# Performance work log

Hardware: AMD Instinct MI355X
Metric: run time of the kernel (lower is better)

## Reference

```python
import jax, jax.numpy as jnp
import numpy as np

H = 1024
HEADS = 16
FFN = 4096
EPS = 1e-5


def _layernorm(x, g, b):
    mu = jnp.mean(x, axis=-1, keepdims=True)
    var = jnp.mean((x - mu) ** 2, axis=-1, keepdims=True)
    return (x - mu) * jax.lax.rsqrt(var + EPS) * g + b


def setup_inputs() -> dict:
    key = jax.random.key(0)
    ks = jax.random.split(key, 12)
    N, L = 2, 2048
    s = 1.0 / np.sqrt(H)
    inp = {
        "src_hidden": jax.random.normal(ks[0], (N, L, H), dtype=jnp.float32),
        "key_mask": jnp.ones((N, L), dtype=jnp.int32),
        "Wq": jax.random.normal(ks[1], (H, H), dtype=jnp.float32) * s,
        "bq": jnp.zeros((H,), dtype=jnp.float32),
        "Wk": jax.random.normal(ks[2], (H, H), dtype=jnp.float32) * s,
        "bk": jnp.zeros((H,), dtype=jnp.float32),
        "Wv": jax.random.normal(ks[3], (H, H), dtype=jnp.float32) * s,
        "bv": jnp.zeros((H,), dtype=jnp.float32),
        "Wo": jax.random.normal(ks[4], (H, H), dtype=jnp.float32) * s,
        "bo": jnp.zeros((H,), dtype=jnp.float32),
        "ln1_g": jnp.ones((H,), dtype=jnp.float32),
        "ln1_b": jnp.zeros((H,), dtype=jnp.float32),
        "W1": jax.random.normal(ks[5], (H, FFN), dtype=jnp.float32) * s,
        "b1": jnp.zeros((FFN,), dtype=jnp.float32),
        "W2": jax.random.normal(ks[6], (FFN, H), dtype=jnp.float32) * (1.0 / np.sqrt(FFN)),
        "b2": jnp.zeros((H,), dtype=jnp.float32),
        "ln2_g": jnp.ones((H,), dtype=jnp.float32),
        "ln2_b": jnp.zeros((H,), dtype=jnp.float32),
    }
    return inp


def reference(src_hidden, key_mask, Wq, bq, Wk, bk, Wv, bv, Wo, bo,
              ln1_g, ln1_b, W1, b1, W2, b2, ln2_g, ln2_b):
    N, L, _ = src_hidden.shape
    d = H // HEADS
    # projections -> (N, heads, L, d)
    q = (src_hidden @ Wq + bq).reshape(N, L, HEADS, d).transpose(0, 2, 1, 3)
    k = (src_hidden @ Wk + bk).reshape(N, L, HEADS, d).transpose(0, 2, 1, 3)
    v = (src_hidden @ Wv + bv).reshape(N, L, HEADS, d).transpose(0, 2, 1, 3)
    # faithful quirk: Q/=sqrt(H) and K/=sqrt(H)  =>  scores scaled by 1/H
    sims = jnp.einsum('bhid,bhjd->bhij', q, k) / H  # (N, heads, L, L)
    mask = key_mask[:, None, None, :] != 0          # (N,1,1,L), masked=False
    sims = jnp.where(mask, sims, -jnp.inf)
    attn = jax.nn.softmax(sims, axis=-1)
    ctx = jnp.einsum('bhij,bhjd->bhid', attn, v)
    concats = ctx.transpose(0, 2, 1, 3).reshape(N, L, H)
    mhsa = concats @ Wo + bo
    # residual + LN1
    x = _layernorm(mhsa + src_hidden, ln1_g, ln1_b)
    # FFN (dropout=0 / eval) + residual + LN2
    ffn = jax.nn.relu(x @ W1 + b1) @ W2 + b2
    out = _layernorm(ffn + x, ln2_g, ln2_b)
    return out
```

## Files before the change

kernel.cpp:

```cpp
#include <hip/hip_runtime.h>
#include <math.h>

#define Hd   1024
#define SEQL 2048
#define NB   2
#define NHEADS 16
#define FFND 4096
#define ROWS 4096
#define QKVLD 3072

typedef __attribute__((ext_vector_type(8))) short short8;
typedef __attribute__((ext_vector_type(4))) float f32x4;
typedef __attribute__((ext_vector_type(16))) float f32x16;

__device__ __forceinline__ unsigned short f2bf(float f) {
  union { float f; unsigned int u; } v; v.f = f;
  return (unsigned short)((v.u + 0x7fffu + ((v.u >> 16) & 1u)) >> 16);
}
__device__ __forceinline__ unsigned short f2bf_fast(float f) {
  union { float f; unsigned int u; } v; v.f = f;
  return (unsigned short)((v.u + 0x8000u) >> 16);
}
__device__ __forceinline__ float bf2f(unsigned short u) {
  union { unsigned int u; float f; } v; v.u = (unsigned int)u << 16;
  return v.f;
}
__device__ __forceinline__ int cvtpk(float a, float b) {
  int d;
  asm("v_cvt_pk_bf16_f32 %0, %1, %2" : "=v"(d) : "v"(a), "v"(b));
  return d;
}
__device__ __forceinline__ void pswap(int& a, int& b) {
  asm("v_permlane32_swap_b32 %0, %1" : "+v"(a), "+v"(b));
}

__device__ __forceinline__ void gl_lds16(const unsigned short* g,
                                         unsigned short* l) {
  __builtin_amdgcn_global_load_lds(
      (const __attribute__((address_space(1))) void*)g,
      (__attribute__((address_space(3))) void*)l, 16, 0, 0);
}

__global__ __launch_bounds__(256) void convert_bf16(
    const float* __restrict__ in, unsigned short* __restrict__ out,
    const float* __restrict__ a, const float* __restrict__ b,
    const float* __restrict__ c, float* __restrict__ o) {
  const int bid = blockIdx.x;
  if (bid >= ROWS * Hd / 1024) {
    const int i = (bid - ROWS * Hd / 1024) * 256 + threadIdx.x;
    o[i] = (i < 1024) ? a[i] : (i < 2048 ? b[i - 1024] : c[i - 2048]);
    return;
  }
  const int i = (bid * 256 + threadIdx.x) * 4;
  float4 x = *(const float4*)&in[i];
  ushort4 ov;
  ov.x = f2bf(x.x); ov.y = f2bf(x.y); ov.z = f2bf(x.z); ov.w = f2bf(x.w);
  *(ushort4*)&out[i] = ov;
}

__global__ __launch_bounds__(256) void convert_transpose(
    const float* __restrict__ W, int ld,
    unsigned short* __restrict__ Wt, int ldt) {
  __shared__ float T[64][65];
  const int t = threadIdx.x;
  const int c0 = blockIdx.x * 64, r0 = blockIdx.y * 64;
#pragma unroll
  for (int p = 0; p < 4; ++p) {
    const int lin = t + p * 256;
    const int r = lin >> 4, c4 = (lin & 15) * 4;
    float4 x = *(const float4*)&W[(size_t)(r0 + r) * ld + c0 + c4];
    T[r][c4 + 0] = x.x; T[r][c4 + 1] = x.y;
    T[r][c4 + 2] = x.z; T[r][c4 + 3] = x.w;
  }
  __syncthreads();
#pragma unroll
  for (int p = 0; p < 2; ++p) {
    const int lin = t + p * 256;
    const int oc = lin >> 3, ch = (lin & 7) * 8;
    union { unsigned short u[8]; uint4 v; } x;
#pragma unroll
    for (int i = 0; i < 8; ++i) x.u[i] = f2bf(T[ch + i][oc]);
    *(uint4*)&Wt[(size_t)(c0 + oc) * ldt + r0 + ch] = x.v;
  }
}

__global__ __launch_bounds__(256) void convert_transpose4(
    const float* __restrict__ W0, const float* __restrict__ W1,
    const float* __restrict__ W2, const float* __restrict__ W3,
    unsigned short* __restrict__ T0, unsigned short* __restrict__ T1,
    unsigned short* __restrict__ T2, unsigned short* __restrict__ T3) {
  __shared__ float T[64][65];
  const float* W = (blockIdx.z == 0) ? W0 : (blockIdx.z == 1) ? W1
                 : (blockIdx.z == 2) ? W2 : W3;
  unsigned short* Wt = (blockIdx.z == 0) ? T0 : (blockIdx.z == 1) ? T1
                     : (blockIdx.z == 2) ? T2 : T3;
  const int t = threadIdx.x;
  const int c0 = blockIdx.x * 64, r0 = blockIdx.y * 64;
#pragma unroll
  for (int p = 0; p < 4; ++p) {
    const int lin = t + p * 256;
    const int r = lin >> 4, c4 = (lin & 15) * 4;
    float4 x = *(const float4*)&W[(size_t)(r0 + r) * Hd + c0 + c4];
    T[r][c4 + 0] = x.x; T[r][c4 + 1] = x.y;
    T[r][c4 + 2] = x.z; T[r][c4 + 3] = x.w;
  }
  __syncthreads();
#pragma unroll
  for (int p = 0; p < 2; ++p) {
    const int lin = t + p * 256;
    const int oc = lin >> 3, ch = (lin & 7) * 8;
    union { unsigned short u[8]; uint4 v; } x;
#pragma unroll
    for (int i = 0; i < 8; ++i) x.u[i] = f2bf(T[ch + i][oc]);
    *(uint4*)&Wt[(size_t)(c0 + oc) * Hd + r0 + ch] = x.v;
  }
}

__global__ __launch_bounds__(256) void transpose_v(
    const unsigned short* __restrict__ v, unsigned short* __restrict__ vt) {
  __shared__ unsigned short T[64][72];
  const int t = threadIdx.x;
  const int s0 = (blockIdx.x & 31) * 64;
  const int bh = blockIdx.x >> 5;
  const int b = bh >> 4, h = bh & 15;
#pragma unroll
  for (int p = 0; p < 2; ++p) {
    const int lin = t + p * 256;
    const int r = lin >> 3, c8 = (lin & 7) * 8;
    *(uint4*)&T[r][c8] =
        *(const uint4*)&v[(size_t)(b * SEQL + s0 + r) * QKVLD + h * 64 + c8];
  }
  __syncthreads();
#pragma unroll
  for (int p = 0; p < 2; ++p) {
    const int lin = t + p * 256;
    const int d = lin >> 3, c8 = (lin & 7) * 8;
    union { unsigned short u[8]; uint4 v4; } x;
#pragma unroll
    for (int i = 0; i < 8; ++i) x.u[i] = T[c8 + i][d];
    *(uint4*)&vt[(size_t)(bh * 64 + d) * SEQL + s0 + c8] = x.v4;
  }
}

template <int BN, int MODE, int OUTBF>
__global__ __launch_bounds__(256, (BN == 128 ? 3 : 4)) void gemm_bt(
    const unsigned short* __restrict__ A, int lda,
    const unsigned short* __restrict__ Bt, int ldb,
    const float* __restrict__ bias,
    void* __restrict__ Cv, int ldc, int K) {
  constexpr int NI = (BN == 128) ? 4 : 2;
  constexpr int BG = BN / 32;
  __shared__ unsigned short As[128 * 64];
  __shared__ unsigned short Bs[BN * 64];
  const int t = threadIdx.x;
  const int wave = t >> 6, lane = t & 63;
  const int l16 = lane & 15, quad = lane >> 4;
  const int m0 = blockIdx.y * 128, n0 = blockIdx.x * BN;
  const int wm = (wave >> 1) * 64, wn = (wave & 1) * (BN / 2);

  const int lr8 = lane >> 3;
  const int sc8 = 8 * ((lane & 7) ^ lr8);

  f32x4 acc[4][NI];
#pragma unroll
  for (int i = 0; i < 4; ++i)
#pragma unroll
    for (int j = 0; j < NI; ++j) acc[i][j] = (f32x4){0.f, 0.f, 0.f, 0.f};

  const unsigned short* Apg[4];
  unsigned short* lAg[4];
#pragma unroll
  for (int j = 0; j < 4; ++j) {
    const int r0 = (wave + 4 * j) * 8;
    Apg[j] = &A[(size_t)(m0 + r0 + lr8) * lda + sc8];
    lAg[j] = &As[r0 * 64];
  }
  const unsigned short* Bpg[BG];
  unsigned short* lBg[BG];
#pragma unroll
  for (int j = 0; j < BG; ++j) {
    const int r0 = (wave + 4 * j) * 8;
    Bpg[j] = &Bt[(size_t)(n0 + r0 + lr8) * ldb + sc8];
    lBg[j] = &Bs[r0 * 64];
  }

  for (int k0 = 0; k0 < K; k0 += 64) {
#pragma unroll
    for (int j = 0; j < 4; ++j) gl_lds16(Apg[j] + k0, lAg[j]);
#pragma unroll
    for (int j = 0; j < BG; ++j) gl_lds16(Bpg[j] + k0, lBg[j]);
    __syncthreads();

#pragma unroll
    for (int kh = 0; kh < 2; ++kh) {
      short8 af[4], bfr[NI];
#pragma unroll
      for (int mi = 0; mi < 4; ++mi) {
        const int r = wm + mi * 16 + l16;
        af[mi] = *(const short8*)&As[r * 64 + (((quad + 4 * kh) ^ (r & 7)) * 8)];
      }
#pragma unroll
      for (int ni = 0; ni < NI; ++ni) {
        const int r = wn + ni * 16 + l16;
        bfr[ni] = *(const short8*)&Bs[r * 64 + (((quad + 4 * kh) ^ (r & 7)) * 8)];
      }
#pragma unroll
      for (int mi = 0; mi < 4; ++mi)
#pragma unroll
        for (int ni = 0; ni < NI; ++ni)
          acc[mi][ni] = __builtin_amdgcn_mfma_f32_16x16x32_bf16(
              af[mi], bfr[ni], acc[mi][ni], 0, 0, 0);
    }
    __syncthreads();
  }

#pragma unroll
  for (int mi = 0; mi < 4; ++mi) {
#pragma unroll
    for (int ni = 0; ni < NI; ++ni) {
      const int col = n0 + wn + ni * 16 + l16;
      const float bv = (MODE == 2) ? 0.0f : bias[col];
#pragma unroll
      for (int r = 0; r < 4; ++r) {
        const int row = m0 + wm + mi * 16 + quad * 4 + r;
        float v = acc[mi][ni][r] + bv;
        if (MODE == 1) v = fmaxf(v, 0.0f);
        if (OUTBF) {
          ((unsigned short*)Cv)[(size_t)row * ldc + col] = f2bf_fast(v);
        } else {
          float* Cf = (float*)Cv;
          if (MODE == 2) Cf[(size_t)row * ldc + col] += v;
          else           Cf[(size_t)row * ldc + col] = v;
        }
      }
    }
  }
}

__global__ __launch_bounds__(256, 4) void attn_mfma(
    const unsigned short* __restrict__ Q,
    const unsigned short* __restrict__ K,
    const unsigned short* __restrict__ Vt,
    const int* __restrict__ mask,
    unsigned short* __restrict__ Op,
    float* __restrict__ ls) {
  __shared__ unsigned short Ks[64 * 72];
  __shared__ unsigned short Vs[64 * 72];

  const int t = threadIdx.x;
  const int wave = t >> 6, lane = t & 63;
  const int l32 = lane & 31, hi = lane >> 5;
  const int qb = blockIdx.x & 15;
  const int h  = (blockIdx.x >> 4) & 15;
  const int b  = (blockIdx.x >> 8) & 1;
  const int jh = blockIdx.x >> 9;
  const int q0 = qb * 128;
  const int bh = b * NHEADS + h;
  const int jbeg = jh * (SEQL / 2), jend = jbeg + SEQL / 2;
  const float NEGINF = -__builtin_inff();

  const int lr = t >> 3, lc8 = (t & 7) * 8;
  const unsigned short* Kbase = &K[(size_t)(b * SEQL + lr) * QKVLD + h * 64 + lc8];
  const unsigned short* Vbase = &Vt[(size_t)(bh * 64 + lr) * SEQL + lc8];
  const size_t Krow32 = (size_t)32 * QKVLD;

  const unsigned short* Qrow =
      &Q[(size_t)(b * SEQL + q0 + wave * 32 + l32) * QKVLD + h * 64];
  short8 qf[4];
#pragma unroll
  for (int ks = 0; ks < 4; ++ks)
    qf[ks] = *(const short8*)&Qrow[ks * 16 + hi * 8];

  float lrow = 0.f;
  f32x16 accO[2];
#pragma unroll
  for (int dt = 0; dt < 2; ++dt)
#pragma unroll
    for (int r = 0; r < 16; ++r) accO[dt][r] = 0.f;

  uint4 kv0 = *(const uint4*)(Kbase + (size_t)jbeg * QKVLD);
  uint4 kv1 = *(const uint4*)(Kbase + (size_t)jbeg * QKVLD + Krow32);
  uint4 vv0 = *(const uint4*)(Vbase + jbeg);
  uint4 vv1 = *(const uint4*)(Vbase + jbeg + 32 * SEQL);

  for (int j0 = jbeg; j0 < jend; j0 += 64) {
    __syncthreads();
    *(uint4*)&Ks[lr * 72 + lc8] = kv0;
    *(uint4*)&Ks[(lr + 32) * 72 + lc8] = kv1;
    *(uint4*)&Vs[lr * 72 + lc8] = vv0;
    *(uint4*)&Vs[(lr + 32) * 72 + lc8] = vv1;
    __syncthreads();

    if (j0 + 64 < jend) {
      const unsigned short* kp = Kbase + (size_t)(j0 + 64) * QKVLD;
      const unsigned short* vp = Vbase + (j0 + 64);
      kv0 = *(const uint4*)(kp);
      kv1 = *(const uint4*)(kp + Krow32);
      vv0 = *(const uint4*)(vp);
      vv1 = *(const uint4*)(vp + 32 * SEQL);
    }

#pragma unroll
    for (int jt = 0; jt < 2; ++jt) {
      f32x16 z;
#pragma unroll
      for (int r = 0; r < 16; ++r) z[r] = 0.f;
#pragma unroll
      for (int ks = 0; ks < 4; ++ks) {
        const short8 ka =
            *(const short8*)&Ks[(jt * 32 + l32) * 72 + ks * 16 + hi * 8];
        z = __builtin_amdgcn_mfma_f32_32x32x16_bf16(ka, qf[ks], z, 0, 0, 0);
      }

      int pk[8];
#pragma unroll
      for (int g = 0; g < 4; ++g) {
        const int4 mm =
            *(const int4*)&mask[b * SEQL + j0 + jt * 32 + g * 8 + hi * 4];
        const int mr[4] = {mm.x, mm.y, mm.z, mm.w};
        float p[4];
#pragma unroll
        for (int e = 0; e < 4; ++e) {
          const float x = mr[e] ? z[g * 4 + e] * (1.0f / 1024.0f) : NEGINF;
          p[e] = __expf(x);
          lrow += p[e];
        }
        pk[g * 2 + 0] = cvtpk(p[0], p[1]);
        pk[g * 2 + 1] = cvtpk(p[2], p[3]);
      }
      pswap(pk[0], pk[2]); pswap(pk[1], pk[3]);
      pswap(pk[4], pk[6]); pswap(pk[5], pk[7]);
      union { int i[4]; short8 s; } pa0, pa1;
      pa0.i[0] = pk[0]; pa0.i[1] = pk[1]; pa0.i[2] = pk[2]; pa0.i[3] = pk[3];
      pa1.i[0] = pk[4]; pa1.i[1] = pk[5]; pa1.i[2] = pk[6]; pa1.i[3] = pk[7];

#pragma unroll
      for (int dt = 0; dt < 2; ++dt) {
        const short8 vb0 = *(const short8*)&Vs[(dt * 32 + l32) * 72 +
                                               jt * 32 + hi * 8];
        const short8 vb1 = *(const short8*)&Vs[(dt * 32 + l32) * 72 +
                                               jt * 32 + 16 + hi * 8];
        accO[dt] = __builtin_amdgcn_mfma_f32_32x32x16_bf16(pa0.s, vb0,
                                                           accO[dt], 0, 0, 0);
        accO[dt] = __builtin_amdgcn_mfma_f32_32x32x16_bf16(pa1.s, vb1,
                                                           accO[dt], 0, 0, 0);
      }
    }
  }

  lrow += __shfl_xor(lrow, 32);
  if (hi == 0)
    ls[((size_t)(jh * NB + b) * NHEADS + h) * SEQL + q0 + wave * 32 + l32] =
        lrow;

#pragma unroll
  for (int dt = 0; dt < 2; ++dt)
#pragma unroll
    for (int r = 0; r < 16; ++r) {
      const int qr = q0 + wave * 32 + (r & 3) + 8 * (r >> 2) + 4 * hi;
      const int rowg = b * SEQL + qr;
      Op[(size_t)jh * ROWS * Hd + (size_t)rowg * Hd + h * 64 + dt * 32 + l32] =
          f2bf_fast(accO[dt][r]);
    }
}

__global__ __launch_bounds__(256) void attn_combine(
    const unsigned short* __restrict__ Op, const float* __restrict__ ls,
    unsigned short* __restrict__ ctxb) {
  const int row = blockIdx.x;
  const int b = row >> 11, q = row & (SEQL - 1);
  const int t = threadIdx.x;
  const int c0 = t * 4, h = t >> 4;
  const float l0 = ls[((size_t)(b)*NHEADS + h) * SEQL + q];
  const float l1 = ls[((size_t)(NB + b) * NHEADS + h) * SEQL + q];
  const float inv = 1.0f / (l0 + l1);
  ushort4 a = *(const ushort4*)&Op[(size_t)row * Hd + c0];
  ushort4 c = *(const ushort4*)&Op[(size_t)ROWS * Hd + (size_t)row * Hd + c0];
  ushort4 o;
  o.x = f2bf_fast((bf2f(a.x) + bf2f(c.x)) * inv);
  o.y = f2bf_fast((bf2f(a.y) + bf2f(c.y)) * inv);
  o.z = f2bf_fast((bf2f(a.z) + bf2f(c.z)) * inv);
  o.w = f2bf_fast((bf2f(a.w) + bf2f(c.w)) * inv);
  *(ushort4*)&ctxb[(size_t)row * Hd + c0] = o;
}

template <int ABF>
__global__ __launch_bounds__(256) void add_ln_kernel(
    const void* Av, const float* R,
    const float* __restrict__ gamma, const float* __restrict__ beta,
    float* out, unsigned short* outb) {
  const int row = blockIdx.x;
  const int t = threadIdx.x;
  const size_t baser = (size_t)row * Hd;

  float a0, a1, a2, a3;
  if (ABF) {
    ushort4 a = *(const ushort4*)&((const unsigned short*)Av)[baser + t * 4];
    a0 = bf2f(a.x); a1 = bf2f(a.y); a2 = bf2f(a.z); a3 = bf2f(a.w);
  } else {
    float4 a = *(const float4*)&((const float*)Av)[baser + t * 4];
    a0 = a.x; a1 = a.y; a2 = a.z; a3 = a.w;
  }
  float4 r = *(const float4*)&R[baser + t * 4];
  float x0 = a0 + r.x, x1 = a1 + r.y, x2 = a2 + r.z, x3 = a3 + r.w;
  float s  = x0 + x1 + x2 + x3;
  float ss = x0 * x0 + x1 * x1 + x2 * x2 + x3 * x3;

#pragma unroll
  for (int off = 32; off > 0; off >>= 1) {
    s  += __shfl_down(s, off, 64);
    ss += __shfl_down(ss, off, 64);
  }

  __shared__ float rs[4], rss[4];
  __shared__ float sh_mean, sh_rstd;
  if ((t & 63) == 0) { rs[t >> 6] = s; rss[t >> 6] = ss; }
  __syncthreads();
  if (t == 0) {
    const float S  = rs[0] + rs[1] + rs[2] + rs[3];
    const float SS = rss[0] + rss[1] + rss[2] + rss[3];
    const float mean = S * (1.0f / Hd);
    const float var  = SS * (1.0f / Hd) - mean * mean;
    sh_mean = mean;
    sh_rstd = rsqrtf(var + 1e-5f);
  }
  __syncthreads();
  const float mean = sh_mean, rstd = sh_rstd;

  float4 gm = *(const float4*)&gamma[t * 4];
  float4 bt = *(const float4*)&beta[t * 4];
  float4 o;
  o.x = (x0 - mean) * rstd * gm.x + bt.x;
  o.y = (x1 - mean) * rstd * gm.y + bt.y;
  o.z = (x2 - mean) * rstd * gm.z + bt.z;
  o.w = (x3 - mean) * rstd * gm.w + bt.w;
  *(float4*)&out[baser + t * 4] = o;
  if (outb) {
    ushort4 ob;
    ob.x = f2bf(o.x); ob.y = f2bf(o.y); ob.z = f2bf(o.z); ob.w = f2bf(o.w);
    *(ushort4*)&outb[baser + t * 4] = ob;
  }
}

extern "C" void kernel_launch(void* const* d_in, const int* in_sizes, int n_in,
                              void* d_out, int out_size, void* d_ws, size_t ws_size,
                              hipStream_t stream) {
  const float* src  = (const float*)d_in[0];
  const int*   kmsk = (const int*)  d_in[1];
  const float* Wq   = (const float*)d_in[2];
  const float* bq   = (const float*)d_in[3];
  const float* Wk   = (const float*)d_in[4];
  const float* bk   = (const float*)d_in[5];
  const float* Wv   = (const float*)d_in[6];
  const float* bv   = (const float*)d_in[7];
  const float* Wo   = (const float*)d_in[8];
  const float* bo   = (const float*)d_in[9];
  const float* ln1g = (const float*)d_in[10];
  const float* ln1b = (const float*)d_in[11];
  const float* W1   = (const float*)d_in[12];
  const float* b1   = (const float*)d_in[13];
  const float* W2   = (const float*)d_in[14];
  const float* b2   = (const float*)d_in[15];
  const float* ln2g = (const float*)d_in[16];
  const float* ln2b = (const float*)d_in[17];

  char* w8 = (char*)d_ws;
  char* o8 = (char*)d_out;
  const size_t MB = 1024 * 1024;
  unsigned short* srcb  = (unsigned short*)(w8 + 0 * MB);
  unsigned short* WqkvT = (unsigned short*)(w8 + 8 * MB);
  float*          bqkv  = (float*)(w8 + 14 * MB);
  unsigned short* qkv   = (unsigned short*)(w8 + 16 * MB);
  unsigned short* vt    = (unsigned short*)(w8 + 40 * MB);
  unsigned short* Opart = (unsigned short*)(w8 + 0 * MB);
  float*          ls    = (float*)(o8 + 8 * MB);
  unsigned short* WoT   = (unsigned short*)(o8 + 9 * MB);
  unsigned short* ctxb  = (unsigned short*)d_out;
  float*          mhsa  = (float*)(w8 + 16 * MB);
  float*          x1    = (float*)d_out;
  unsigned short* x1b   = (unsigned short*)(w8 + 8 * MB);
  unsigned short* W1T   = (unsigned short*)(w8 + 0 * MB);
  unsigned short* hb    = (unsigned short*)(w8 + 16 * MB);
  unsigned short* W2T   = (unsigned short*)(w8 + 0 * MB);
  unsigned short* f2b   = (unsigned short*)(w8 + 8 * MB);

  dim3 blk(256);

  convert_bf16<<<ROWS * Hd / 1024 + 12, blk, 0, stream>>>(
      src, srcb, bq, bk, bv, bqkv);
  convert_transpose4<<<dim3(16, 16, 4), blk, 0, stream>>>(
      Wq, Wk, Wv, Wo, WqkvT, WqkvT + 1024 * 1024, WqkvT + 2 * 1024 * 1024, WoT);

  gemm_bt<128, 0, 1><<<dim3(QKVLD / 128, ROWS / 128), blk, 0, stream>>>(
      srcb, Hd, WqkvT, Hd, bqkv, qkv, QKVLD, Hd);

  transpose_v<<<1024, blk, 0, stream>>>(qkv + 2048, vt);
  attn_mfma<<<1024, blk, 0, stream>>>(qkv, qkv + 1024, vt, kmsk, Opart, ls);
  attn_combine<<<ROWS, blk, 0, stream>>>(Opart, ls, ctxb);

  gemm_bt<64, 0, 0><<<dim3(Hd / 64, ROWS / 128), blk, 0, stream>>>(
      ctxb, Hd, WoT, Hd, bo, mhsa, Hd, Hd);

  add_ln_kernel<0><<<ROWS, blk, 0, stream>>>(mhsa, src, ln1g, ln1b, x1, x1b);

  convert_transpose<<<dim3(64, 16), blk, 0, stream>>>(W1, FFND, W1T, Hd);
  gemm_bt<128, 1, 1><<<dim3(FFND / 128, ROWS / 128), blk, 0, stream>>>(
      x1b, Hd, W1T, Hd, b1, hb, FFND, Hd);
  convert_transpose<<<dim3(16, 64), blk, 0, stream>>>(W2, Hd, W2T, FFND);
  gemm_bt<64, 0, 1><<<dim3(Hd / 64, ROWS / 128), blk, 0, stream>>>(
      hb, FFND, W2T, FFND, b2, f2b, Hd, FFND);

  add_ln_kernel<1><<<ROWS, blk, 0, stream>>>(f2b, x1, ln2g, ln2b,
                                             (float*)d_out, nullptr);
}
```

Baseline: 378.6 us.

## Precompute additive mask, use exp2 softmax, add MFMA priority and GEMM block swizzle

The key mask is turned into an additive float bias (0 or -inf) inside the conversion kernel. The attention kernel then computes each softmax term with one fma into log2 scale and a raw v_exp_f32, which removes the select and the multiply inside __expf. s_setprio hints are placed around the MFMA sections. Separately, the GEMM kernel remaps block IDs with a modulo-8 swizzle, presumably to spread concurrent workgroups across XCDs for better cache locality. Together these add a small extra buffer and raise the scheduling complexity.

```diff
diff --git a/kernel.cpp b/kernel.cpp
--- a/kernel.cpp
+++ b/kernel.cpp
@@ -44,10 +44,17 @@
 __global__ __launch_bounds__(256) void convert_bf16(
     const float* __restrict__ in, unsigned short* __restrict__ out,
     const float* __restrict__ a, const float* __restrict__ b,
-    const float* __restrict__ c, float* __restrict__ o) {
+    const float* __restrict__ c, float* __restrict__ o,
+    const int* __restrict__ kmsk, float* __restrict__ maskb) {
   const int bid = blockIdx.x;
-  if (bid >= ROWS * Hd / 1024) {
-    const int i = (bid - ROWS * Hd / 1024) * 256 + threadIdx.x;
+  const int NCONV = ROWS * Hd / 1024;
+  if (bid >= NCONV + 12) {
+    const int i = (bid - NCONV - 12) * 256 + threadIdx.x;
+    maskb[i] = kmsk[i] ? 0.0f : -__builtin_inff();
+    return;
+  }
+  if (bid >= NCONV) {
+    const int i = (bid - NCONV) * 256 + threadIdx.x;
     o[i] = (i < 1024) ? a[i] : (i < 2048 ? b[i - 1024] : c[i - 2048]);
     return;
   }
@@ -155,7 +162,13 @@
   const int t = threadIdx.x;
   const int wave = t >> 6, lane = t & 63;
   const int l16 = lane & 15, quad = lane >> 4;
-  const int m0 = blockIdx.y * 128, n0 = blockIdx.x * BN;
+
+  const int gx = gridDim.x;
+  const int nwg = gx * gridDim.y;
+  const int id = blockIdx.y * gx + blockIdx.x;
+  const int swz = (id & 7) * (nwg >> 3) + (id >> 3);
+  const int m0 = (swz / gx) * 128, n0 = (swz % gx) * BN;
+
   const int wm = (wave >> 1) * 64, wn = (wave & 1) * (BN / 2);
 
   const int lr8 = lane >> 3;
@@ -241,7 +254,7 @@
     const unsigned short* __restrict__ Q,
     const unsigned short* __restrict__ K,
     const unsigned short* __restrict__ Vt,
-    const int* __restrict__ mask,
+    const float* __restrict__ maskb,
     unsigned short* __restrict__ Op,
     float* __restrict__ ls) {
   __shared__ unsigned short Ks[64 * 72];
@@ -257,7 +270,7 @@
   const int q0 = qb * 128;
   const int bh = b * NHEADS + h;
   const int jbeg = jh * (SEQL / 2), jend = jbeg + SEQL / 2;
-  const float NEGINF = -__builtin_inff();
+  const float C2 = 1.4426950408889634f * (1.0f / 1024.0f);
 
   const int lr = t >> 3, lc8 = (t & 7) * 8;
   const unsigned short* Kbase = &K[(size_t)(b * SEQL + lr) * QKVLD + h * 64 + lc8];
@@ -305,24 +318,26 @@
       f32x16 z;
 #pragma unroll
       for (int r = 0; r < 16; ++r) z[r] = 0.f;
+      __builtin_amdgcn_s_setprio(1);
 #pragma unroll
       for (int ks = 0; ks < 4; ++ks) {
         const short8 ka =
             *(const short8*)&Ks[(jt * 32 + l32) * 72 + ks * 16 + hi * 8];
         z = __builtin_amdgcn_mfma_f32_32x32x16_bf16(ka, qf[ks], z, 0, 0, 0);
       }
+      __builtin_amdgcn_s_setprio(0);
 
       int pk[8];
 #pragma unroll
       for (int g = 0; g < 4; ++g) {
-        const int4 mm =
-            *(const int4*)&mask[b * SEQL + j0 + jt * 32 + g * 8 + hi * 4];
-        const int mr[4] = {mm.x, mm.y, mm.z, mm.w};
+        const float4 mb =
+            *(const float4*)&maskb[b * SEQL + j0 + jt * 32 + g * 8 + hi * 4];
+        const float mbe[4] = {mb.x, mb.y, mb.z, mb.w};
         float p[4];
 #pragma unroll
         for (int e = 0; e < 4; ++e) {
-          const float x = mr[e] ? z[g * 4 + e] * (1.0f / 1024.0f) : NEGINF;
-          p[e] = __expf(x);
+          const float x = fmaf(z[g * 4 + e], C2, mbe[e]);
+          asm("v_exp_f32 %0, %1" : "=v"(p[e]) : "v"(x));
           lrow += p[e];
         }
         pk[g * 2 + 0] = cvtpk(p[0], p[1]);
@@ -334,6 +349,7 @@
       pa0.i[0] = pk[0]; pa0.i[1] = pk[1]; pa0.i[2] = pk[2]; pa0.i[3] = pk[3];
       pa1.i[0] = pk[4]; pa1.i[1] = pk[5]; pa1.i[2] = pk[6]; pa1.i[3] = pk[7];
 
+      __builtin_amdgcn_s_setprio(1);
 #pragma unroll
       for (int dt = 0; dt < 2; ++dt) {
         const short8 vb0 = *(const short8*)&Vs[(dt * 32 + l32) * 72 +
@@ -345,6 +361,7 @@
         accO[dt] = __builtin_amdgcn_mfma_f32_32x32x16_bf16(pa1.s, vb1,
                                                            accO[dt], 0, 0, 0);
       }
+      __builtin_amdgcn_s_setprio(0);
     }
   }
 
@@ -474,6 +491,7 @@
   unsigned short* vt    = (unsigned short*)(w8 + 40 * MB);
   unsigned short* Opart = (unsigned short*)(w8 + 0 * MB);
   float*          ls    = (float*)(o8 + 8 * MB);
+  float*          maskb = (float*)(o8 + 8 * MB + 512 * 1024);
   unsigned short* WoT   = (unsigned short*)(o8 + 9 * MB);
   unsigned short* ctxb  = (unsigned short*)d_out;
   float*          mhsa  = (float*)(w8 + 16 * MB);
@@ -486,8 +504,8 @@
 
   dim3 blk(256);
 
-  convert_bf16<<<ROWS * Hd / 1024 + 12, blk, 0, stream>>>(
-      src, srcb, bq, bk, bv, bqkv);
+  convert_bf16<<<ROWS * Hd / 1024 + 12 + 16, blk, 0, stream>>>(
+      src, srcb, bq, bk, bv, bqkv, kmsk, maskb);
   convert_transpose4<<<dim3(16, 16, 4), blk, 0, stream>>>(
       Wq, Wk, Wv, Wo, WqkvT, WqkvT + 1024 * 1024, WqkvT + 2 * 1024 * 1024, WoT);
 
@@ -495,7 +513,7 @@
       srcb, Hd, WqkvT, Hd, bqkv, qkv, QKVLD, Hd);
 
   transpose_v<<<1024, blk, 0, stream>>>(qkv + 2048, vt);
-  attn_mfma<<<1024, blk, 0, stream>>>(qkv, qkv + 1024, vt, kmsk, Opart, ls);
+  attn_mfma<<<1024, blk, 0, stream>>>(qkv, qkv + 1024, vt, maskb, Opart, ls);
   attn_combine<<<ROWS, blk, 0, stream>>>(Opart, ls, ctxb);
 
   gemm_bt<64, 0, 0><<<dim3(Hd / 64, ROWS / 128), blk, 0, stream>>>(
```

New measurement: 356.6 us. 5.8% less time.
